# Performance work log

Hardware: AMD Instinct MI355X
Metric: run time of the kernel (lower is better)

The kernel has to match this reference:

```python
import jax, jax.numpy as jnp
import numpy as np

B, H, W, C = 4, 224, 224, 256
HEADS = 8
WIN = 7
N = WIN * WIN  # 49 tokens per window
MLP_HID = 4 * C
EPS = 1e-5


def _rel_index(w):
    coords = np.stack(np.meshgrid(np.arange(w), np.arange(w), indexing='ij'))  # (2,w,w)
    cf = coords.reshape(2, -1)                       # (2, w*w)
    rc = cf[:, :, None] - cf[:, None, :]             # (2, N, N)
    rc = rc.transpose(1, 2, 0).astype(np.int64)      # (N, N, 2)
    rc[:, :, 0] += w - 1
    rc[:, :, 1] += w - 1
    rc[:, :, 0] *= 2 * w - 1
    return jnp.asarray(rc.sum(-1), dtype=jnp.int32)  # (N, N)


def setup_inputs() -> dict:
    key = jax.random.key(0)
    ks = jax.random.split(key, 6)
    std = 0.02
    return {
        'x': jax.random.normal(ks[0], (B, H, W, C), dtype=jnp.float32),
        'norm1_g': jnp.ones((C,), jnp.float32),
        'norm1_b': jnp.zeros((C,), jnp.float32),
        'qkv_w': jax.random.normal(ks[1], (3 * C, C), jnp.float32) * std,
        'qkv_b': jnp.zeros((3 * C,), jnp.float32),
        'bias_table': jax.random.normal(ks[2], ((2 * WIN - 1) ** 2, HEADS), jnp.float32) * std,
        'proj_w': jax.random.normal(ks[3], (C, C), jnp.float32) * std,
        'proj_b': jnp.zeros((C,), jnp.float32),
        'norm2_g': jnp.ones((C,), jnp.float32),
        'norm2_b': jnp.zeros((C,), jnp.float32),
        'fc1_w': jax.random.normal(ks[4], (MLP_HID, C), jnp.float32) * std,
        'fc1_b': jnp.zeros((MLP_HID,), jnp.float32),
        'fc2_w': jax.random.normal(ks[5], (C, MLP_HID), jnp.float32) * std,
        'fc2_b': jnp.zeros((C,), jnp.float32),
        'rel_index': _rel_index(WIN),
    }


def _layernorm(x, g, b):
    mu = jnp.mean(x, axis=-1, keepdims=True)
    var = jnp.mean(jnp.square(x - mu), axis=-1, keepdims=True)
    return (x - mu) * jax.lax.rsqrt(var + EPS) * g + b


def reference(x, norm1_g, norm1_b, qkv_w, qkv_b, bias_table, proj_w, proj_b,
              norm2_g, norm2_b, fc1_w, fc1_b, fc2_w, fc2_b, rel_index):
    Bc, Hc, Wc, Cc = x.shape
    d = Cc // HEADS
    scale = d ** -0.5
    nh, nw = Hc // WIN, Wc // WIN

    shortcut = x
    h = _layernorm(x, norm1_g, norm1_b)

    # window_partition: (B,H,W,C) -> (B*nW, N, C)
    wins = h.reshape(Bc, nh, WIN, nw, WIN, Cc).transpose(0, 1, 3, 2, 4, 5)
    wins = wins.reshape(-1, N, Cc)

    # qkv projection and split into heads
    qkv = wins @ qkv_w.T + qkv_b                                  # (Bw, N, 3C)
    qkv = qkv.reshape(-1, N, 3, HEADS, d).transpose(2, 0, 3, 1, 4)  # (3, Bw, h, N, d)
    q, k, v = qkv[0], qkv[1], qkv[2]

    attn = jnp.einsum('bhnd,bhmd->bhnm', q, k) * scale            # (Bw, h, N, N)
    bias = bias_table[rel_index.reshape(-1)].reshape(N, N, HEADS).transpose(2, 0, 1)
    attn = jax.nn.softmax(attn + bias[None], axis=-1)

    o = jnp.einsum('bhnm,bhmd->bhnd', attn, v)                    # (Bw, h, N, d)
    o = o.transpose(0, 2, 1, 3).reshape(-1, N, Cc)
    o = o @ proj_w.T + proj_b

    # window_reverse: (B*nW, N, C) -> (B,H,W,C)
    o = o.reshape(Bc, nh, nw, WIN, WIN, Cc).transpose(0, 1, 3, 2, 4, 5)
    o = o.reshape(Bc, Hc, Wc, Cc)

    x = shortcut + o
    h2 = _layernorm(x, norm2_g, norm2_b)
    m = jax.nn.gelu(h2 @ fc1_w.T + fc1_b, approximate=False) @ fc2_w.T + fc2_b
    return x + m
```

## Files before the change

### kernel.cpp

```cpp
#include <hip/hip_runtime.h>

typedef unsigned short u16;
typedef __bf16 bf16x8 __attribute__((ext_vector_type(8)));
typedef float f32x4 __attribute__((ext_vector_type(4)));

#define TOKENS 200704
#define QK_ELEMS 51380224UL

__device__ __forceinline__ u16 f2b(float f) {
    __bf16 h = (__bf16)f;
    return __builtin_bit_cast(u16, h);
}

#define GLDS(g, l) __builtin_amdgcn_global_load_lds( \
    (const __attribute__((address_space(1))) void*)(g), \
    (__attribute__((address_space(3))) void*)(l), 16, 0, 0)

#define MFMA __builtin_amdgcn_mfma_f32_16x16x32_bf16

template<int EPI>
__global__ __launch_bounds__(512, 2)
void gemm256(const u16* __restrict__ A, const u16* __restrict__ W,
             const float* __restrict__ bias, int nt, int K,
             u16* __restrict__ outb, float* __restrict__ outf,
             const float* __restrict__ res)
{
    __shared__ u16 As[2][256 * 64];
    __shared__ u16 Bs[2][256 * 64];
    const int tid  = threadIdx.x;
    const int wave = tid >> 6, lane = tid & 63;

    const int nwg = gridDim.x, bidO = blockIdx.x;
    const int qq = nwg >> 3, rr = nwg & 7;
    const int xcd = bidO & 7, idxx = bidO >> 3;
    const int bid = (xcd < rr) ? (xcd * (qq + 1) + idxx)
                               : (rr * (qq + 1) + (xcd - rr) * qq + idxx);

    const int bm = bid / nt, bn = bid % nt;
    const long m0 = (long)bm * 256;
    const int  n0 = bn * 256;
    const int wr = wave >> 2, wc = wave & 3;
    const int lr = lane & 15, lg = lane >> 4;
    const int crow   = lane >> 3;
    const int ccol_s = ((lane & 7) ^ crow) * 8;
    const int swz    = (lr & 7) * 8;

    f32x4 acc[8][4] = {};

    auto stage = [&](int buf, int k0) {
#pragma unroll
        for (int p = 0; p < 4; ++p) {
            const int i = p * 8 + wave;
            const int row = i * 8 + crow;
            GLDS(A + (m0 + row) * (long)K + k0 + ccol_s, &As[buf][i * 512]);
            GLDS(W + (long)(n0 + row) * K + k0 + ccol_s, &Bs[buf][i * 512]);
        }
    };

    auto compute = [&](int buf) {
        bf16x8 bfr[2][4];
#pragma unroll
        for (int kk2 = 0; kk2 < 2; ++kk2)
#pragma unroll
            for (int fn = 0; fn < 4; ++fn)
                bfr[kk2][fn] = *reinterpret_cast<const bf16x8*>(
                    &Bs[buf][(wc * 64 + fn * 16 + lr) * 64 + ((kk2 * 32 + lg * 8) ^ swz)]);
        bf16x8 aq[2][2], an[2][2];
#pragma unroll
        for (int p = 0; p < 2; ++p)
#pragma unroll
            for (int kk2 = 0; kk2 < 2; ++kk2)
                aq[p][kk2] = *reinterpret_cast<const bf16x8*>(
                    &As[buf][(wr * 128 + p * 16 + lr) * 64 + ((kk2 * 32 + lg * 8) ^ swz)]);
#pragma unroll
        for (int q = 0; q < 4; ++q) {
            bf16x8 (&cur)[2][2] = (q & 1) ? an : aq;
            bf16x8 (&nxt)[2][2] = (q & 1) ? aq : an;
            if (q < 3) {
#pragma unroll
                for (int p = 0; p < 2; ++p)
#pragma unroll
                    for (int kk2 = 0; kk2 < 2; ++kk2)
                        nxt[p][kk2] = *reinterpret_cast<const bf16x8*>(
                            &As[buf][(wr * 128 + (2 * (q + 1) + p) * 16 + lr) * 64 + ((kk2 * 32 + lg * 8) ^ swz)]);
            }
            __builtin_amdgcn_s_setprio(1);
#pragma unroll
            for (int p = 0; p < 2; ++p)
#pragma unroll
                for (int kk2 = 0; kk2 < 2; ++kk2)
#pragma unroll
                    for (int fn = 0; fn < 4; ++fn)
                        acc[2 * q + p][fn] = MFMA(cur[p][kk2], bfr[kk2][fn], acc[2 * q + p][fn], 0, 0, 0);
            __builtin_amdgcn_s_setprio(0);
        }
    };

    const int nk = K >> 6;
    stage(0, 0);
    stage(1, 64);
    int k = 128;
    for (int t = 0; t < nk - 1; ++t) {
        asm volatile("s_waitcnt vmcnt(8)" ::: "memory");
        __builtin_amdgcn_s_barrier();
        __builtin_amdgcn_sched_barrier(0);
        compute(t & 1);
        __builtin_amdgcn_s_barrier();
        __builtin_amdgcn_sched_barrier(0);
        if (t + 2 < nk) {
            stage(t & 1, k); k += 64;
            __builtin_amdgcn_sched_barrier(0);
        }
    }
    asm volatile("s_waitcnt vmcnt(0)" ::: "memory");
    __builtin_amdgcn_s_barrier();
    __builtin_amdgcn_sched_barrier(0);
    compute((nk - 1) & 1);

#pragma unroll
    for (int fm = 0; fm < 8; ++fm) {
#pragma unroll
        for (int r = 0; r < 4; ++r) {
            const long m = m0 + wr * 128 + fm * 16 + lg * 4 + r;
            size_t mpart = 0;
            if (EPI == 0) {
                const int mm = (int)m;
                const int b = mm / 50176;
                const int rem = mm % 50176;
                const int y = rem / 224, x = rem % 224;
                const int win = (b * 32 + y / 7) * 32 + x / 7;
                const int pos = (y % 7) * 7 + (x % 7);
                mpart = (size_t)win * 12544 + (size_t)pos * 32;
            }
#pragma unroll
            for (int fn = 0; fn < 4; ++fn) {
                const int n = n0 + wc * 64 + fn * 16 + lr;
                const float v = acc[fm][fn][r];
                if (EPI == 0) {
                    const int sec = n >> 8, hd = (n >> 5) & 7, d = n & 31;
                    const float sc = (sec == 0) ? 0.17677669529663687f : 1.0f;
                    outb[sec * QK_ELEMS + mpart + hd * 1568 + d] = f2b((v + bias[n]) * sc);
                } else if (EPI == 1) {
                    outf[m * 256 + n] = v + bias[n] + res[m * 256 + n];
                } else if (EPI == 2) {
                    const float t = v + bias[n];
                    const float s = t * (1.5957691216f + 0.07135481627f * t * t);
                    const float g = t * __builtin_amdgcn_rcpf(1.0f + __expf(-s));
                    outb[m * 1024 + n] = f2b(g);
                } else {
                    outf[m * 256 + n] += v + bias[n];
                }
            }
        }
    }
}

__global__ __launch_bounds__(256)
void layernorm_k(const float* __restrict__ in, const float* __restrict__ g,
                 const float* __restrict__ bb, u16* __restrict__ out)
{
    const int token = blockIdx.x * 4 + (threadIdx.x >> 6);
    const int lane = threadIdx.x & 63;
    const float4 v = *reinterpret_cast<const float4*>(in + (size_t)token * 256 + lane * 4);
    float s  = v.x + v.y + v.z + v.w;
    float s2 = v.x * v.x + v.y * v.y + v.z * v.z + v.w * v.w;
#pragma unroll
    for (int m = 1; m < 64; m <<= 1) { s += __shfl_xor(s, m); s2 += __shfl_xor(s2, m); }
    const float mu  = s * (1.0f / 256.0f);
    const float var = s2 * (1.0f / 256.0f) - mu * mu;
    const float rs  = rsqrtf(var + 1e-5f);
    const float4 gv = *reinterpret_cast<const float4*>(g + lane * 4);
    const float4 bv = *reinterpret_cast<const float4*>(bb + lane * 4);
    ushort4 o;
    o.x = f2b((v.x - mu) * rs * gv.x + bv.x);
    o.y = f2b((v.y - mu) * rs * gv.y + bv.y);
    o.z = f2b((v.z - mu) * rs * gv.z + bv.z);
    o.w = f2b((v.w - mu) * rs * gv.w + bv.w);
    *reinterpret_cast<ushort4*>(out + (size_t)token * 256 + lane * 4) = o;
}

__global__ __launch_bounds__(256)
void attn_win(const u16* __restrict__ qkv, const float* __restrict__ biasF,
              u16* __restrict__ outb)
{
    __shared__ u16 plds[4][64 * 72];
    __shared__ u16 vlds[4][32 * 72];
    const int wave = threadIdx.x >> 6, lane = threadIdx.x & 63;
    const int pair = blockIdx.x * 4 + wave;
    const int head = pair & 7, win = pair >> 3;
    const int lr = lane & 15, lg = lane >> 4;

    const u16* Q  = qkv + (size_t)pair * 1568;
    const u16* Kp = qkv + QK_ELEMS + (size_t)pair * 1568;
    const u16* Vp = qkv + 2 * QK_ELEMS + (size_t)pair * 1568;

    u16* vl = &vlds[wave][0];
#pragma unroll
    for (int it = 0; it < 8; ++it) {
        const int idx = it * 64 + lane;
        if (idx < 480) vl[(idx / 15) * 72 + 49 + idx % 15] = 0;
    }
#pragma unroll
    for (int it = 0; it < 4; ++it) {
        const int idx = it * 64 + lane;
        if (idx < 196) {
            const int pos = idx >> 2, dc = idx & 3;
            const uint4 vv = *reinterpret_cast<const uint4*>(Vp + pos * 32 + dc * 8);
            u16* dst = vl + (dc * 8) * 72 + pos;
            dst[0 * 72] = (u16)vv.x;  dst[1 * 72] = (u16)(vv.x >> 16);
            dst[2 * 72] = (u16)vv.y;  dst[3 * 72] = (u16)(vv.y >> 16);
            dst[4 * 72] = (u16)vv.z;  dst[5 * 72] = (u16)(vv.z >> 16);
            dst[6 * 72] = (u16)vv.w;  dst[7 * 72] = (u16)(vv.w >> 16);
        }
    }

    bf16x8 qf[4], kf[4];
#pragma unroll
    for (int f = 0; f < 4; ++f) {
        int n = f * 16 + lr; n = n > 48 ? 48 : n;
        qf[f] = *reinterpret_cast<const bf16x8*>(Q  + n * 32 + lg * 8);
        kf[f] = *reinterpret_cast<const bf16x8*>(Kp + n * 32 + lg * 8);
    }
    f32x4 s[4][4] = {};
#pragma unroll
    for (int fm = 0; fm < 4; ++fm)
#pragma unroll
        for (int fn = 0; fn < 4; ++fn)
            s[fm][fn] = MFMA(qf[fm], kf[fn], s[fm][fn], 0, 0, 0);

    const float* bh = biasF + head * 2401;
    u16* pl = &plds[wave][0];
#pragma unroll
    for (int fm = 0; fm < 4; ++fm) {
#pragma unroll
        for (int r = 0; r < 4; ++r) {
            const int row = fm * 16 + lg * 4 + r;
            const int brow = row > 48 ? 48 : row;
            float v[4];
#pragma unroll
            for (int fn = 0; fn < 4; ++fn) {
                const int col = fn * 16 + lr;
                const float bval = bh[brow * 49 + (col > 48 ? 48 : col)];
                v[fn] = (col > 48) ? -3.0e38f : (s[fm][fn][r] + bval);
            }
            float mx = fmaxf(fmaxf(v[0], v[1]), fmaxf(v[2], v[3]));
#pragma unroll
            for (int d = 1; d < 16; d <<= 1) mx = fmaxf(mx, __shfl_xor(mx, d));
            float p[4], sum = 0.f;
#pragma unroll
            for (int fn = 0; fn < 4; ++fn) {
                const int col = fn * 16 + lr;
                p[fn] = (col <= 48) ? __expf(v[fn] - mx) : 0.f;
                sum += p[fn];
            }
#pragma unroll
            for (int d = 1; d < 16; d <<= 1) sum += __shfl_xor(sum, d);
            const float rinv = __builtin_amdgcn_rcpf(sum);
#pragma unroll
            for (int fn = 0; fn < 4; ++fn)
                pl[row * 72 + fn * 16 + lr] = f2b(p[fn] * rinv);
        }
    }
    __syncthreads();

    f32x4 o[4][2] = {};
#pragma unroll
    for (int kc = 0; kc < 2; ++kc) {
        bf16x8 vf[2];
#pragma unroll
        for (int f2 = 0; f2 < 2; ++f2)
            vf[f2] = *reinterpret_cast<const bf16x8*>(vl + (f2 * 16 + lr) * 72 + kc * 32 + lg * 8);
#pragma unroll
        for (int fm = 0; fm < 4; ++fm) {
            const bf16x8 pa = *reinterpret_cast<const bf16x8*>(pl + (fm * 16 + lr) * 72 + kc * 32 + lg * 8);
#pragma unroll
            for (int f2 = 0; f2 < 2; ++f2)
                o[fm][f2] = MFMA(pa, vf[f2], o[fm][f2], 0, 0, 0);
        }
    }

    const int b = win >> 10, rem = win & 1023, wy = rem >> 5, wx = rem & 31;
#pragma unroll
    for (int fm = 0; fm < 4; ++fm) {
#pragma unroll
        for (int r = 0; r < 4; ++r) {
            const int tok = fm * 16 + lg * 4 + r;
            if (tok > 48) continue;
            const int y = wy * 7 + tok / 7, xx = wx * 7 + tok % 7;
            const size_t mrow = ((size_t)(b * 224 + y)) * 224 + xx;
#pragma unroll
            for (int f2 = 0; f2 < 2; ++f2)
                outb[mrow * 256 + head * 32 + f2 * 16 + lr] = f2b(o[fm][f2][r]);
        }
    }
}

__global__ __launch_bounds__(256)
void cvt_w(const float* __restrict__ qw, const float* __restrict__ pw,
           const float* __restrict__ f1, const float* __restrict__ f2,
           u16* __restrict__ outw)
{
    const int t = blockIdx.x * 256 + threadIdx.x;
    float v;
    if (t < 196608) v = qw[t];
    else if (t < 262144) v = pw[t - 196608];
    else if (t < 524288) v = f1[t - 262144];
    else v = f2[t - 524288];
    outw[t] = f2b(v);
}

__global__ __launch_bounds__(256)
void bias_pre(const float* __restrict__ btab, const int* __restrict__ relidx,
              float* __restrict__ biasF)
{
    const int t = blockIdx.x * 256 + threadIdx.x;
    if (t >= 19208) return;
    const int head = t / 2401, ij = t % 2401;
    biasF[t] = btab[relidx[ij] * 8 + head];
}

extern "C" void kernel_launch(void* const* d_in, const int* in_sizes, int n_in,
                              void* d_out, int out_size, void* d_ws, size_t ws_size,
                              hipStream_t stream)
{
    const float* x      = (const float*)d_in[0];
    const float* n1g    = (const float*)d_in[1];
    const float* n1b    = (const float*)d_in[2];
    const float* qkv_w  = (const float*)d_in[3];
    const float* qkv_b  = (const float*)d_in[4];
    const float* btab   = (const float*)d_in[5];
    const float* proj_w = (const float*)d_in[6];
    const float* proj_b = (const float*)d_in[7];
    const float* n2g    = (const float*)d_in[8];
    const float* n2b    = (const float*)d_in[9];
    const float* fc1_w  = (const float*)d_in[10];
    const float* fc1_b  = (const float*)d_in[11];
    const float* fc2_w  = (const float*)d_in[12];
    const float* fc2_b  = (const float*)d_in[13];
    const int*   relidx = (const int*)d_in[14];
    float* out = (float*)d_out;

    char* ws = (char*)d_ws;
    u16*   wbf   = (u16*)ws;
    float* biasF = (float*)(ws + 1572864);
    u16*   hbuf  = (u16*)(ws + 1650688);
    u16*   rbuf  = (u16*)(ws + 1650688 + 102760448);
    const size_t r_avail = ws_size - (1650688 + 102760448);

    const u16* Wq  = wbf;
    const u16* Wp  = wbf + 196608;
    const u16* Wf1 = wbf + 262144;
    const u16* Wf2 = wbf + 524288;

    cvt_w<<<3072, 256, 0, stream>>>(qkv_w, proj_w, fc1_w, fc2_w, wbf);
    bias_pre<<<76, 256, 0, stream>>>(btab, relidx, biasF);
    layernorm_k<<<50176, 256, 0, stream>>>(x, n1g, n1b, hbuf);

    gemm256<0><<<784 * 3, 512, 0, stream>>>(hbuf, Wq, qkv_b, 3, 256, rbuf, nullptr, nullptr);
    attn_win<<<8192, 256, 0, stream>>>(rbuf, biasF, hbuf);
    gemm256<1><<<784, 512, 0, stream>>>(hbuf, Wp, proj_b, 1, 256, nullptr, out, x);
    layernorm_k<<<50176, 256, 0, stream>>>(out, n2g, n2b, hbuf);

    long rows_cap = (long)(r_avail / 2048);
    long rows_per = (rows_cap / 256) * 256;
    if (rows_per > TOKENS) rows_per = TOKENS;
    if (rows_per < 256) rows_per = 256;
    for (long r0 = 0; r0 < TOKENS; r0 += rows_per) {
        const long rows = (TOKENS - r0 < rows_per) ? (TOKENS - r0) : rows_per;
        gemm256<2><<<(int)((rows / 256) * 4), 512, 0, stream>>>(
            hbuf + r0 * 256, Wf1, fc1_b, 4, 256, rbuf, nullptr, nullptr);
        gemm256<3><<<(int)(rows / 256), 512, 0, stream>>>(
            rbuf, Wf2, fc2_b, 1, 1024, nullptr, out + r0 * 256, nullptr);
    }
}
```

Baseline: 1.135 ms.

## Fuse LayerNorm2 into proj GEMM epilogue and batch-chunk QKV/attention

The proj GEMM epilogue now writes the residual sum and also computes LayerNorm2 in place. Each 256-row tile does a cross-wave reduction through shared memory, which removes the separate layernorm kernel and its full read and write pass over activations. The QKV GEMM and window attention are now launched per batch image, so each slice of the qkv intermediate is consumed soon after it is written and is more likely to stay in the last-level cache. The MLP row chunk size is also fixed to larger chunks. The costs are a barrier plus extra shared memory and registers in the proj epilogue, and more kernel launches.

```diff
diff --git a/kernel.cpp b/kernel.cpp
--- a/kernel.cpp
+++ b/kernel.cpp
@@ -21,9 +21,11 @@
 template<int EPI>
 __global__ __launch_bounds__(512, 2)
 void gemm256(const u16* __restrict__ A, const u16* __restrict__ W,
-             const float* __restrict__ bias, int nt, int K,
+             const float* __restrict__ bias, int nt, int K, long moff,
              u16* __restrict__ outb, float* __restrict__ outf,
-             const float* __restrict__ res)
+             const float* __restrict__ res,
+             const float* __restrict__ g2, const float* __restrict__ b2,
+             u16* __restrict__ h2o)
 {
     __shared__ u16 As[2][256 * 64];
     __shared__ u16 Bs[2][256 * 64];
@@ -117,38 +119,86 @@
     __builtin_amdgcn_sched_barrier(0);
     compute((nk - 1) & 1);
 
-#pragma unroll
-    for (int fm = 0; fm < 8; ++fm) {
-#pragma unroll
-        for (int r = 0; r < 4; ++r) {
-            const long m = m0 + wr * 128 + fm * 16 + lg * 4 + r;
-            size_t mpart = 0;
-            if (EPI == 0) {
-                const int mm = (int)m;
-                const int b = mm / 50176;
-                const int rem = mm % 50176;
-                const int y = rem / 224, x = rem % 224;
-                const int win = (b * 32 + y / 7) * 32 + x / 7;
-                const int pos = (y % 7) * 7 + (x % 7);
-                mpart = (size_t)win * 12544 + (size_t)pos * 32;
-            }
-#pragma unroll
-            for (int fn = 0; fn < 4; ++fn) {
-                const int n = n0 + wc * 64 + fn * 16 + lr;
-                const float v = acc[fm][fn][r];
+    if constexpr (EPI == 1) {
+        __shared__ float red[2][256][4];
+        float g2c[4], b2c[4];
+#pragma unroll
+        for (int fn = 0; fn < 4; ++fn) {
+            const int n = wc * 64 + fn * 16 + lr;
+            g2c[fn] = g2[n]; b2c[fn] = b2[n];
+        }
+#pragma unroll
+        for (int fm = 0; fm < 8; ++fm) {
+#pragma unroll
+            for (int r = 0; r < 4; ++r) {
+                const long m = m0 + wr * 128 + fm * 16 + lg * 4 + r;
+                float s = 0.f, s2 = 0.f;
+#pragma unroll
+                for (int fn = 0; fn < 4; ++fn) {
+                    const int n = wc * 64 + fn * 16 + lr;
+                    const float x2 = acc[fm][fn][r] + bias[n] + res[m * 256 + n];
+                    acc[fm][fn][r] = x2;
+                    outf[m * 256 + n] = x2;
+                    s += x2; s2 += x2 * x2;
+                }
+#pragma unroll
+                for (int d = 1; d < 16; d <<= 1) { s += __shfl_xor(s, d); s2 += __shfl_xor(s2, d); }
+                if (lr == 0) {
+                    const int tok = wr * 128 + fm * 16 + lg * 4 + r;
+                    red[0][tok][wc] = s; red[1][tok][wc] = s2;
+                }
+            }
+        }
+        __syncthreads();
+#pragma unroll
+        for (int fm = 0; fm < 8; ++fm) {
+#pragma unroll
+            for (int r = 0; r < 4; ++r) {
+                const int tok = wr * 128 + fm * 16 + lg * 4 + r;
+                const float s  = red[0][tok][0] + red[0][tok][1] + red[0][tok][2] + red[0][tok][3];
+                const float q  = red[1][tok][0] + red[1][tok][1] + red[1][tok][2] + red[1][tok][3];
+                const float mu = s * 0.00390625f;
+                const float rs = rsqrtf(q * 0.00390625f - mu * mu + 1e-5f);
+                const long m = m0 + tok;
+#pragma unroll
+                for (int fn = 0; fn < 4; ++fn) {
+                    const int n = wc * 64 + fn * 16 + lr;
+                    h2o[m * 256 + n] = f2b((acc[fm][fn][r] - mu) * rs * g2c[fn] + b2c[fn]);
+                }
+            }
+        }
+    } else {
+#pragma unroll
+        for (int fm = 0; fm < 8; ++fm) {
+#pragma unroll
+            for (int r = 0; r < 4; ++r) {
+                const long m = m0 + wr * 128 + fm * 16 + lg * 4 + r;
+                size_t mpart = 0;
                 if (EPI == 0) {
-                    const int sec = n >> 8, hd = (n >> 5) & 7, d = n & 31;
-                    const float sc = (sec == 0) ? 0.17677669529663687f : 1.0f;
-                    outb[sec * QK_ELEMS + mpart + hd * 1568 + d] = f2b((v + bias[n]) * sc);
-                } else if (EPI == 1) {
-                    outf[m * 256 + n] = v + bias[n] + res[m * 256 + n];
-                } else if (EPI == 2) {
-                    const float t = v + bias[n];
-                    const float s = t * (1.5957691216f + 0.07135481627f * t * t);
-                    const float g = t * __builtin_amdgcn_rcpf(1.0f + __expf(-s));
-                    outb[m * 1024 + n] = f2b(g);
-                } else {
-                    outf[m * 256 + n] += v + bias[n];
+                    const int gm = (int)(m + moff);
+                    const int b = gm / 50176;
+                    const int rem = gm % 50176;
+                    const int y = rem / 224, x = rem % 224;
+                    const int win = (b * 32 + y / 7) * 32 + x / 7;
+                    const int pos = (y % 7) * 7 + (x % 7);
+                    mpart = (size_t)win * 12544 + (size_t)pos * 32;
+                }
+#pragma unroll
+                for (int fn = 0; fn < 4; ++fn) {
+                    const int n = n0 + wc * 64 + fn * 16 + lr;
+                    const float v = acc[fm][fn][r];
+                    if (EPI == 0) {
+                        const int sec = n >> 8, hd = (n >> 5) & 7, d = n & 31;
+                        const float sc = (sec == 0) ? 0.17677669529663687f : 1.0f;
+                        outb[sec * QK_ELEMS + mpart + hd * 1568 + d] = f2b((v + bias[n]) * sc);
+                    } else if (EPI == 2) {
+                        const float t = v + bias[n];
+                        const float s = t * (1.5957691216f + 0.07135481627f * t * t);
+                        const float g = t * __builtin_amdgcn_rcpf(1.0f + __expf(-s));
+                        outb[m * 1024 + n] = f2b(g);
+                    } else {
+                        outf[m * 256 + n] += v + bias[n];
+                    }
                 }
             }
         }
@@ -181,12 +231,12 @@
 
 __global__ __launch_bounds__(256)
 void attn_win(const u16* __restrict__ qkv, const float* __restrict__ biasF,
-              u16* __restrict__ outb)
+              u16* __restrict__ outb, int pair0)
 {
     __shared__ u16 plds[4][64 * 72];
     __shared__ u16 vlds[4][32 * 72];
     const int wave = threadIdx.x >> 6, lane = threadIdx.x & 63;
-    const int pair = blockIdx.x * 4 + wave;
+    const int pair = pair0 + blockIdx.x * 4 + wave;
     const int head = pair & 7, win = pair >> 3;
     const int lr = lane & 15, lg = lane >> 4;
 
@@ -356,20 +406,23 @@
     bias_pre<<<76, 256, 0, stream>>>(btab, relidx, biasF);
     layernorm_k<<<50176, 256, 0, stream>>>(x, n1g, n1b, hbuf);
 
-    gemm256<0><<<784 * 3, 512, 0, stream>>>(hbuf, Wq, qkv_b, 3, 256, rbuf, nullptr, nullptr);
-    attn_win<<<8192, 256, 0, stream>>>(rbuf, biasF, hbuf);
-    gemm256<1><<<784, 512, 0, stream>>>(hbuf, Wp, proj_b, 1, 256, nullptr, out, x);
-    layernorm_k<<<50176, 256, 0, stream>>>(out, n2g, n2b, hbuf);
-
-    long rows_cap = (long)(r_avail / 2048);
-    long rows_per = (rows_cap / 256) * 256;
-    if (rows_per > TOKENS) rows_per = TOKENS;
-    if (rows_per < 256) rows_per = 256;
+    for (int b = 0; b < 4; ++b) {
+        gemm256<0><<<588, 512, 0, stream>>>(hbuf + (size_t)b * 50176 * 256, Wq, qkv_b,
+                                            3, 256, (long)b * 50176,
+                                            rbuf, nullptr, nullptr, nullptr, nullptr, nullptr);
+        attn_win<<<2048, 256, 0, stream>>>(rbuf, biasF, hbuf, b * 8192);
+    }
+
+    gemm256<1><<<784, 512, 0, stream>>>(hbuf, Wp, proj_b, 1, 256, 0,
+                                        nullptr, out, x, n2g, n2b, hbuf);
+
+    long rows_per = 100352;
+    if ((long)(r_avail / 2048) < rows_per) rows_per = 50176;
     for (long r0 = 0; r0 < TOKENS; r0 += rows_per) {
         const long rows = (TOKENS - r0 < rows_per) ? (TOKENS - r0) : rows_per;
         gemm256<2><<<(int)((rows / 256) * 4), 512, 0, stream>>>(
-            hbuf + r0 * 256, Wf1, fc1_b, 4, 256, rbuf, nullptr, nullptr);
+            hbuf + r0 * 256, Wf1, fc1_b, 4, 256, 0, rbuf, nullptr, nullptr, nullptr, nullptr, nullptr);
         gemm256<3><<<(int)(rows / 256), 512, 0, stream>>>(
-            rbuf, Wf2, fc2_b, 1, 1024, nullptr, out + r0 * 256, nullptr);
-    }
-}
+            rbuf, Wf2, fc2_b, 1, 1024, 0, nullptr, out + r0 * 256, nullptr, nullptr, nullptr, nullptr);
+    }
+}
```

After: 1.192 ms. 1.05x slower.
